# Kernel tuning notes

Hardware: AMD Instinct MI355X
Metric: run time of the kernel (lower is better)

Reference implementation:

```python
import jax, jax.numpy as jnp
import numpy as np

L = 4            # l1 = l2 = lambd = 4
M = 2 * L + 1    # 9 m-channels
N = 4096         # environment pairs
D = 256          # feature channels
K = 100          # number of nonzero real-CG terms


def setup_inputs() -> dict:
    key = jax.random.key(0)
    k1, k2, k3, k4, k5, k6 = jax.random.split(key, 6)
    X1 = jax.random.normal(k1, (M, N, D), dtype=jnp.float32)
    X2 = jax.random.normal(k2, (M, N, D), dtype=jnp.float32)
    m1_aligned = jax.random.randint(k3, (K,), 0, M)
    m2_aligned = jax.random.randint(k4, (K,), 0, M)
    mu = jnp.sort(jax.random.randint(k5, (K,), 0, M))  # appended in mu order in the torch init
    multipliers = jax.random.normal(k6, (K,), dtype=jnp.float32)
    return {"X1": X1, "X2": X2, "m1_aligned": m1_aligned,
            "m2_aligned": m2_aligned, "mu": mu, "multipliers": multipliers}


def reference(X1, X2, m1_aligned, m2_aligned, mu, multipliers):
    # gather along m-dim, elementwise multiply by CG multipliers  -> [K, N, D]
    contributions = X1[m1_aligned] * X2[m2_aligned] * multipliers[:, None, None]
    # scatter-add into the 2*lambd+1 output channels (mu is sorted)
    result = jax.ops.segment_sum(contributions, mu, num_segments=M,
                                 indices_are_sorted=True)
    return result  # [2*lambd+1, N, D]
```

## Files before the change

kernel.cpp:

```cpp
#include <hip/hip_runtime.h>


#define M_CH 9
#define TILE 512
#define THREADS 128
#define PLAN_PAD 128

typedef const void __attribute__((address_space(1))) * gcptr;
typedef void       __attribute__((address_space(3))) * lsptr;

__global__ __launch_bounds__(128) void prep_kernel(
    const int* __restrict__ m1, const int* __restrict__ m2,
    const int* __restrict__ mu, const float* __restrict__ mult,
    int K, int* __restrict__ ws) {
    __shared__ int smu[PLAN_PAD];
    int t = threadIdx.x;
    if (t < K) smu[t] = mu[t];
    __syncthreads();
    int4* plan = (int4*)(ws + 16);
    if (t < K) {
        int4 e;
        e.x = m1[t] * (TILE * 4);
        e.y = (M_CH + m2[t]) * (TILE * 4);
        e.z = __float_as_int(mult[t]);
        e.w = 0;
        plan[t] = e;
    } else if (t < PLAN_PAD) {
        int4 e; e.x = 0; e.y = M_CH * TILE * 4; e.z = 0; e.w = 0;
        plan[t] = e;
    }
    if (t <= M_CH) {
        int c = 0;
        for (int k = 0; k < K; ++k) c += (smu[k] < t) ? 1 : 0;
        ws[t] = c;
    }
}

__global__ __launch_bounds__(THREADS) void cleb_kernel(
    const float* __restrict__ X1, const float* __restrict__ X2,
    const int* __restrict__ ws, float* __restrict__ out, int P) {
    __shared__ float lds[2 * M_CH * TILE];
    const int tid = threadIdx.x;
    const int base = blockIdx.x * TILE;

    const float* src1 = X1 + base + tid * 4;
    const float* src2 = X2 + base + tid * 4;
    #pragma unroll
    for (int m = 0; m < M_CH; ++m) {
        __builtin_amdgcn_global_load_lds((gcptr)(src1 + m * P),
                                         (lsptr)&lds[m * TILE + tid * 4], 16, 0, 0);
        __builtin_amdgcn_global_load_lds((gcptr)(src2 + m * P),
                                         (lsptr)&lds[(M_CH + m) * TILE + tid * 4], 16, 0, 0);
    }

    int seg[M_CH + 1];
    #pragma unroll
    for (int i = 0; i <= M_CH; ++i) seg[i] = ws[i];
    const int4* plan = (const int4*)(ws + 16);

    __syncthreads();

    const char* ldsb = (const char*)lds;
    const int lane_off = tid * 16;
    float* outp = out + base + tid * 4;

    #pragma unroll
    for (int m = 0; m < M_CH; ++m) {
        float4 acc = make_float4(0.f, 0.f, 0.f, 0.f);
        const int s = seg[m], e = seg[m + 1];
        int4 pe = plan[s];
        #pragma unroll 2
        for (int k = s; k < e; ++k) {
            int4 pn = plan[k + 1];
            const float4 a = *(const float4*)(ldsb + pe.x + lane_off);
            const float4 b = *(const float4*)(ldsb + pe.y + lane_off);
            const float c = __int_as_float(pe.z);
            acc.x = fmaf(c * a.x, b.x, acc.x);
            acc.y = fmaf(c * a.y, b.y, acc.y);
            acc.z = fmaf(c * a.z, b.z, acc.z);
            acc.w = fmaf(c * a.w, b.w, acc.w);
            pe = pn;
        }
        *(float4*)(outp + m * P) = acc;
    }
}

extern "C" void kernel_launch(void* const* d_in, const int* in_sizes, int n_in,
                              void* d_out, int out_size, void* d_ws, size_t ws_size,
                              hipStream_t stream) {
    const float* X1   = (const float*)d_in[0];
    const float* X2   = (const float*)d_in[1];
    const int*   m1   = (const int*)d_in[2];
    const int*   m2   = (const int*)d_in[3];
    const int*   mu   = (const int*)d_in[4];
    const float* mult = (const float*)d_in[5];
    float* out = (float*)d_out;
    int*   ws  = (int*)d_ws;

    const int K = in_sizes[2];
    const int P = in_sizes[0] / M_CH;

    prep_kernel<<<1, 128, 0, stream>>>(m1, m2, mu, mult, K, ws);
    cleb_kernel<<<P / TILE, THREADS, 0, stream>>>(X1, X2, ws, out, P);
}
```

Measured before the change: 133.2 us.

## Double-buffer LDS tiles across four tiles per single-wave block

Each block becomes one 64-thread wave that walks four 256-column tiles in turn. It stages the next tile into a second LDS buffer with async global-to-LDS loads while computing the current one. Partial vmcnt waits stand in for block-wide barriers. This aims to hide load latency inside each wave, at the cost of fewer blocks and some reliance on the exact count of outstanding memory operations (vmcnt(18) must match the stores and loads issued).

```diff
diff --git a/kernel.cpp b/kernel.cpp
--- a/kernel.cpp
+++ b/kernel.cpp
@@ -2,8 +2,9 @@
 
 
 #define M_CH 9
-#define TILE 512
-#define THREADS 128
+#define TILE 256
+#define THREADS 64
+#define TPB 4
 #define PLAN_PAD 128
 
 typedef const void __attribute__((address_space(1))) * gcptr;
@@ -36,52 +37,66 @@
     }
 }
 
+__device__ __forceinline__ void stage_tile(float* dst, const float* s1,
+                                           const float* s2, int P, int tid) {
+    #pragma unroll
+    for (int m = 0; m < M_CH; ++m) {
+        __builtin_amdgcn_global_load_lds((gcptr)(s1 + m * P),
+                                         (lsptr)(dst + m * TILE + tid * 4), 16, 0, 0);
+        __builtin_amdgcn_global_load_lds((gcptr)(s2 + m * P),
+                                         (lsptr)(dst + (M_CH + m) * TILE + tid * 4), 16, 0, 0);
+    }
+}
+
 __global__ __launch_bounds__(THREADS) void cleb_kernel(
     const float* __restrict__ X1, const float* __restrict__ X2,
     const int* __restrict__ ws, float* __restrict__ out, int P) {
-    __shared__ float lds[2 * M_CH * TILE];
+    __shared__ float lds[2][2 * M_CH * TILE];
     const int tid = threadIdx.x;
-    const int base = blockIdx.x * TILE;
+    const int base0 = blockIdx.x * (TILE * TPB);
 
-    const float* src1 = X1 + base + tid * 4;
-    const float* src2 = X2 + base + tid * 4;
-    #pragma unroll
-    for (int m = 0; m < M_CH; ++m) {
-        __builtin_amdgcn_global_load_lds((gcptr)(src1 + m * P),
-                                         (lsptr)&lds[m * TILE + tid * 4], 16, 0, 0);
-        __builtin_amdgcn_global_load_lds((gcptr)(src2 + m * P),
-                                         (lsptr)&lds[(M_CH + m) * TILE + tid * 4], 16, 0, 0);
-    }
+    stage_tile(lds[0], X1 + base0 + tid * 4, X2 + base0 + tid * 4, P, tid);
 
     int seg[M_CH + 1];
     #pragma unroll
     for (int i = 0; i <= M_CH; ++i) seg[i] = ws[i];
     const int4* plan = (const int4*)(ws + 16);
-
-    __syncthreads();
-
-    const char* ldsb = (const char*)lds;
     const int lane_off = tid * 16;
-    float* outp = out + base + tid * 4;
 
     #pragma unroll
-    for (int m = 0; m < M_CH; ++m) {
-        float4 acc = make_float4(0.f, 0.f, 0.f, 0.f);
-        const int s = seg[m], e = seg[m + 1];
-        int4 pe = plan[s];
-        #pragma unroll 2
-        for (int k = s; k < e; ++k) {
-            int4 pn = plan[k + 1];
-            const float4 a = *(const float4*)(ldsb + pe.x + lane_off);
-            const float4 b = *(const float4*)(ldsb + pe.y + lane_off);
-            const float c = __int_as_float(pe.z);
-            acc.x = fmaf(c * a.x, b.x, acc.x);
-            acc.y = fmaf(c * a.y, b.y, acc.y);
-            acc.z = fmaf(c * a.z, b.z, acc.z);
-            acc.w = fmaf(c * a.w, b.w, acc.w);
-            pe = pn;
+    for (int t = 0; t < TPB; ++t) {
+        const int base = base0 + t * TILE;
+        if (t + 1 < TPB) {
+            stage_tile(lds[(t + 1) & 1], X1 + base + TILE + tid * 4,
+                       X2 + base + TILE + tid * 4, P, tid);
+            asm volatile("s_waitcnt vmcnt(18)" ::: "memory");
+        } else {
+            asm volatile("s_waitcnt vmcnt(0)" ::: "memory");
         }
-        *(float4*)(outp + m * P) = acc;
+        __builtin_amdgcn_sched_barrier(0);
+
+        const char* ldsb = (const char*)lds[t & 1];
+        float* outp = out + base + tid * 4;
+
+        #pragma unroll
+        for (int m = 0; m < M_CH; ++m) {
+            float4 acc = make_float4(0.f, 0.f, 0.f, 0.f);
+            const int s_ = seg[m], e_ = seg[m + 1];
+            int4 pe = plan[s_];
+            #pragma unroll 4
+            for (int k = s_; k < e_; ++k) {
+                int4 pn = plan[k + 1];
+                const float4 a = *(const float4*)(ldsb + pe.x + lane_off);
+                const float4 b = *(const float4*)(ldsb + pe.y + lane_off);
+                const float c = __int_as_float(pe.z);
+                acc.x = fmaf(c * a.x, b.x, acc.x);
+                acc.y = fmaf(c * a.y, b.y, acc.y);
+                acc.z = fmaf(c * a.z, b.z, acc.z);
+                acc.w = fmaf(c * a.w, b.w, acc.w);
+                pe = pn;
+            }
+            *(float4*)(outp + m * P) = acc;
+        }
     }
 }
 
@@ -101,5 +116,5 @@
     const int P = in_sizes[0] / M_CH;
 
     prep_kernel<<<1, 128, 0, stream>>>(m1, m2, mu, mult, K, ws);
-    cleb_kernel<<<P / TILE, THREADS, 0, stream>>>(X1, X2, ws, out, P);
+    cleb_kernel<<<P / (TILE * TPB), THREADS, 0, stream>>>(X1, X2, ws, out, P);
 }
```

Result: no change. 135.4 us (+1.6%).

## Replace sparse CG plan with dense coefficient tensor and register-resident compute

Applied to the files above, without the earlier changes.

Builds a dense 9x9x9 coupling tensor in the prep kernel and has the main kernel load all X1/X2 channels into registers, computing every pairwise product against the dense coefficients fetched via readlane. This removes LDS staging, the block barrier, and per-term plan loads. In exchange it performs many more FMAs (including zero coefficients), uses heavy register state that limits occupancy, and the prep kernel becomes a serial single-thread loop.

```diff
diff --git a/kernel.cpp b/kernel.cpp
--- a/kernel.cpp
+++ b/kernel.cpp
@@ -2,87 +2,68 @@
 
 
 #define M_CH 9
-#define TILE 512
-#define THREADS 128
-#define PLAN_PAD 128
+#define CSIZE 768
 
-typedef const void __attribute__((address_space(1))) * gcptr;
-typedef void       __attribute__((address_space(3))) * lsptr;
-
-__global__ __launch_bounds__(128) void prep_kernel(
+__global__ __launch_bounds__(64) void prep_kernel(
     const int* __restrict__ m1, const int* __restrict__ m2,
     const int* __restrict__ mu, const float* __restrict__ mult,
-    int K, int* __restrict__ ws) {
-    __shared__ int smu[PLAN_PAD];
-    int t = threadIdx.x;
-    if (t < K) smu[t] = mu[t];
-    __syncthreads();
-    int4* plan = (int4*)(ws + 16);
-    if (t < K) {
-        int4 e;
-        e.x = m1[t] * (TILE * 4);
-        e.y = (M_CH + m2[t]) * (TILE * 4);
-        e.z = __float_as_int(mult[t]);
-        e.w = 0;
-        plan[t] = e;
-    } else if (t < PLAN_PAD) {
-        int4 e; e.x = 0; e.y = M_CH * TILE * 4; e.z = 0; e.w = 0;
-        plan[t] = e;
-    }
-    if (t <= M_CH) {
-        int c = 0;
-        for (int k = 0; k < K; ++k) c += (smu[k] < t) ? 1 : 0;
-        ws[t] = c;
+    int K, float* __restrict__ Cd) {
+    if (threadIdx.x == 0) {
+        for (int i = 0; i < CSIZE; ++i) Cd[i] = 0.f;
+        for (int k = 0; k < K; ++k) {
+            const int idx = (m1[k] * M_CH + m2[k]) * M_CH + mu[k];
+            Cd[idx] += mult[k];
+        }
     }
 }
 
-__global__ __launch_bounds__(THREADS) void cleb_kernel(
+__global__ __launch_bounds__(64) void cleb_dense(
     const float* __restrict__ X1, const float* __restrict__ X2,
-    const int* __restrict__ ws, float* __restrict__ out, int P) {
-    __shared__ float lds[2 * M_CH * TILE];
-    const int tid = threadIdx.x;
-    const int base = blockIdx.x * TILE;
+    const float* __restrict__ Cd, float* __restrict__ out, int P) {
+    const int lane = threadIdx.x;
+    const size_t base = (size_t)blockIdx.x * 256 + (size_t)lane * 4;
 
-    const float* src1 = X1 + base + tid * 4;
-    const float* src2 = X2 + base + tid * 4;
+    float4 x1[M_CH], x2[M_CH];
     #pragma unroll
     for (int m = 0; m < M_CH; ++m) {
-        __builtin_amdgcn_global_load_lds((gcptr)(src1 + m * P),
-                                         (lsptr)&lds[m * TILE + tid * 4], 16, 0, 0);
-        __builtin_amdgcn_global_load_lds((gcptr)(src2 + m * P),
-                                         (lsptr)&lds[(M_CH + m) * TILE + tid * 4], 16, 0, 0);
+        x1[m] = *(const float4*)(X1 + (size_t)m * P + base);
+        x2[m] = *(const float4*)(X2 + (size_t)m * P + base);
     }
 
-    int seg[M_CH + 1];
+    int tab[12];
     #pragma unroll
-    for (int i = 0; i <= M_CH; ++i) seg[i] = ws[i];
-    const int4* plan = (const int4*)(ws + 16);
+    for (int r = 0; r < 12; ++r)
+        tab[r] = ((const int*)Cd)[r * 64 + lane];
 
-    __syncthreads();
-
-    const char* ldsb = (const char*)lds;
-    const int lane_off = tid * 16;
-    float* outp = out + base + tid * 4;
+    float4 acc[M_CH];
+    #pragma unroll
+    for (int m = 0; m < M_CH; ++m) acc[m] = make_float4(0.f, 0.f, 0.f, 0.f);
 
     #pragma unroll
-    for (int m = 0; m < M_CH; ++m) {
-        float4 acc = make_float4(0.f, 0.f, 0.f, 0.f);
-        const int s = seg[m], e = seg[m + 1];
-        int4 pe = plan[s];
-        #pragma unroll 2
-        for (int k = s; k < e; ++k) {
-            int4 pn = plan[k + 1];
-            const float4 a = *(const float4*)(ldsb + pe.x + lane_off);
-            const float4 b = *(const float4*)(ldsb + pe.y + lane_off);
-            const float c = __int_as_float(pe.z);
-            acc.x = fmaf(c * a.x, b.x, acc.x);
-            acc.y = fmaf(c * a.y, b.y, acc.y);
-            acc.z = fmaf(c * a.z, b.z, acc.z);
-            acc.w = fmaf(c * a.w, b.w, acc.w);
-            pe = pn;
+    for (int p1 = 0; p1 < M_CH; ++p1) {
+        #pragma unroll
+        for (int p2 = 0; p2 < M_CH; ++p2) {
+            float4 prod;
+            prod.x = x1[p1].x * x2[p2].x;
+            prod.y = x1[p1].y * x2[p2].y;
+            prod.z = x1[p1].z * x2[p2].z;
+            prod.w = x1[p1].w * x2[p2].w;
+            #pragma unroll
+            for (int m = 0; m < M_CH; ++m) {
+                const int idx = (p1 * M_CH + p2) * M_CH + m;
+                const float c = __int_as_float(
+                    __builtin_amdgcn_readlane(tab[idx >> 6], idx & 63));
+                acc[m].x = fmaf(c, prod.x, acc[m].x);
+                acc[m].y = fmaf(c, prod.y, acc[m].y);
+                acc[m].z = fmaf(c, prod.z, acc[m].z);
+                acc[m].w = fmaf(c, prod.w, acc[m].w);
+            }
         }
-        *(float4*)(outp + m * P) = acc;
     }
+
+    #pragma unroll
+    for (int m = 0; m < M_CH; ++m)
+        *(float4*)(out + (size_t)m * P + base) = acc[m];
 }
 
 extern "C" void kernel_launch(void* const* d_in, const int* in_sizes, int n_in,
@@ -95,11 +76,11 @@
     const int*   mu   = (const int*)d_in[4];
     const float* mult = (const float*)d_in[5];
     float* out = (float*)d_out;
-    int*   ws  = (int*)d_ws;
+    float* Cd  = (float*)d_ws;
 
     const int K = in_sizes[2];
     const int P = in_sizes[0] / M_CH;
 
-    prep_kernel<<<1, 128, 0, stream>>>(m1, m2, mu, mult, K, ws);
-    cleb_kernel<<<P / TILE, THREADS, 0, stream>>>(X1, X2, ws, out, P);
+    prep_kernel<<<1, 64, 0, stream>>>(m1, m2, mu, mult, K, Cd);
+    cleb_dense<<<P / 256, 64, 0, stream>>>(X1, X2, Cd, out, P);
 }
```

Result: slower. 149.8 us (+12.4%).
